# Kernel tuning notes

Measured on AMD Instinct MI355X. Metric: run time of the kernel, lower is better.

Reference implementation:

```python
import jax, jax.numpy as jnp
import numpy as np

N, T, IN, HID, ST, NL, OUT = 256, 2048, 6, 128, 64, 2, 6
LAY = IN + HID  # LMSCCell layer_size = input_size + hidden_size


def setup_inputs() -> dict:
    key = jax.random.key(0)
    ks = jax.random.split(key, 8)

    def w(k, shape, fan_in):
        return jax.random.normal(k, shape, jnp.float32) / np.sqrt(fan_in).astype(np.float32)

    return {
        "X": jax.random.normal(ks[0], (N, T, IN), jnp.float32),
        "H0": jax.random.normal(ks[1], (N, ST), jnp.float32),
        # NL gated layers (layer_size -> layer_size), stored stacked, weights as (in, out)
        "Wg1": w(ks[2], (NL, LAY, LAY), LAY), "bg1": jnp.zeros((NL, LAY), jnp.float32),
        "Wg2": w(ks[3], (NL, LAY, LAY), LAY), "bg2": jnp.zeros((NL, LAY), jnp.float32),
        # final pair: alpha (exp) and beta (tanh), layer_size -> hidden
        "Wa": w(ks[4], (LAY, HID), LAY), "ba": jnp.zeros((HID,), jnp.float32),
        "Wb": w(ks[5], (LAY, HID), LAY), "bb": jnp.zeros((HID,), jnp.float32),
        # hstate: Linear(state_size -> hidden) producing S0
        "Wh": w(ks[6], (ST, HID), ST), "bh": jnp.zeros((HID,), jnp.float32),
        # sstate2: Linear(hidden -> out_size)
        "Wo": w(ks[7], (HID, OUT), HID), "bo": jnp.zeros((OUT,), jnp.float32),
    }


def reference(X, H0, Wg1, bg1, Wg2, bg2, Wa, ba, Wb, bb, Wh, bh, Wo, bo):
    # hstate: initial hidden state for the LMSC recurrence
    S0 = H0 @ Wh + bh  # (N, HID)

    def step(H, x_t):
        # x_t: (N, IN); H: (N, HID)
        norm = jnp.linalg.norm(x_t, axis=1, keepdims=True)  # (N, 1)
        Lv = jnp.concatenate([x_t / norm, H], axis=1)       # (N, LAY)
        for i in range(NL):  # small fixed layer count, structurally distinct weights
            Lv = jnp.tanh(Lv @ Wg1[i] + bg1[i]) * jnp.tanh(Lv @ Wg2[i] + bg2[i])
        alpha = jnp.exp(Lv @ Wa + ba)   # (N, HID)
        beta = jnp.tanh(Lv @ Wb + bb)   # (N, HID)
        Hn = jnp.exp(-alpha * norm) * (H - beta) + beta
        return Hn, Hn

    _, Ys = jax.lax.scan(step, S0, jnp.swapaxes(X, 0, 1))  # (T, N, HID)
    Y = jnp.swapaxes(Ys, 0, 1)  # (N, T, HID)
    return Y @ Wo + bo          # (N, T, OUT)
```

## Files before the change

kernel.cpp:

```cpp
#include <hip/hip_runtime.h>

#define Nb   256
#define Tt   2048
#define INs  6
#define HID  128
#define STs  64
#define LAY  134
#define OUTs 6
#define NPAIR 67
#define NDW  68

typedef _Float16 h2 __attribute__((ext_vector_type(2)));
typedef __fp16  f16x2 __attribute__((ext_vector_type(2)));

__device__ __forceinline__ float exp2_fast(float x) {
#if __has_builtin(__builtin_amdgcn_exp2f)
    return __builtin_amdgcn_exp2f(x);
#else
    return exp2f(x);
#endif
}
__device__ __forceinline__ float rcp_fast(float x) {
#if __has_builtin(__builtin_amdgcn_rcpf)
    return __builtin_amdgcn_rcpf(x);
#else
    return 1.0f / x;
#endif
}
__device__ __forceinline__ float tanh_fast(float x) {
    float e = exp2_fast(x * 2.8853900817779268f);
    return 1.0f - 2.0f * rcp_fast(e + 1.0f);
}
__device__ __forceinline__ unsigned pack2(float a, float b) {
#if __has_builtin(__builtin_amdgcn_cvt_pkrtz)
    union { f16x2 h; unsigned u; } u;
    u.h = __builtin_amdgcn_cvt_pkrtz(a, b);
    return u.u;
#else
    union { h2 h; unsigned u; } u;
    u.h[0] = (_Float16)a; u.h[1] = (_Float16)b;
    return u.u;
#endif
}
__device__ __forceinline__ h2 as_h2(unsigned v) {
    union { unsigned u; h2 h; } u; u.u = v; return u.h;
}
__device__ __forceinline__ float dot2f(h2 a, h2 b, float c) {
#if __has_builtin(__builtin_amdgcn_fdot2)
    union { h2 h; f16x2 f; } ua, ub;
    ua.h = a; ub.h = b;
    return __builtin_amdgcn_fdot2(ua.f, ub.f, c, false);
#else
    return c + (float)a[0] * (float)b[0] + (float)a[1] * (float)b[1];
#endif
}

__device__ __forceinline__ void dotLv2(const unsigned* buf, const h2* w1, const h2* w2,
                                       float b1, float b2, float& o1, float& o2) {
    const uint4* b4 = (const uint4*)buf;
    float a0 = 0.f, a1 = 0.f, a2 = 0.f, a3 = 0.f;
    float c0 = 0.f, c1 = 0.f, c2 = 0.f, c3 = 0.f;
#pragma unroll
    for (int m = 0; m < 17; ++m) {
        uint4 v = b4[m];
        h2 vx = as_h2(v.x), vy = as_h2(v.y), vz = as_h2(v.z), vw = as_h2(v.w);
        a0 = dot2f(vx, w1[4*m+0], a0);  c0 = dot2f(vx, w2[4*m+0], c0);
        a1 = dot2f(vy, w1[4*m+1], a1);  c1 = dot2f(vy, w2[4*m+1], c1);
        a2 = dot2f(vz, w1[4*m+2], a2);  c2 = dot2f(vz, w2[4*m+2], c2);
        a3 = dot2f(vw, w1[4*m+3], a3);  c3 = dot2f(vw, w2[4*m+3], c3);
    }
    o1 = ((a0 + a1) + (a2 + a3)) + b1;
    o2 = ((c0 + c1) + (c2 + c3)) + b2;
}

__device__ __forceinline__ void do_proj(const float* Hrow, const float* wo0, const float* wo1,
                                        const float* bo6, float* outp, int l) {
    float hA = Hrow[2*l], hB = Hrow[2*l+1];
    float r[6];
#pragma unroll
    for (int o = 0; o < 6; ++o) r[o] = hA * wo0[o] + hB * wo1[o];
#pragma unroll
    for (int o = 0; o < 6; ++o) {
#pragma unroll
        for (int k = 1; k < 64; k <<= 1) r[o] += __shfl_xor(r[o], k, 64);
    }
    if (l == 0) {
#pragma unroll
        for (int o = 0; o < 6; ++o) outp[o] = r[o] + bo6[o];
    }
}

__global__ __launch_bounds__(512, 2)
void lmsc_kernel(const float* __restrict__ X,  const float* __restrict__ H0,
                 const float* __restrict__ Wg1, const float* __restrict__ bg1,
                 const float* __restrict__ Wg2, const float* __restrict__ bg2,
                 const float* __restrict__ Wa,  const float* __restrict__ ba,
                 const float* __restrict__ Wb,  const float* __restrict__ bb,
                 const float* __restrict__ Wh,  const float* __restrict__ bh,
                 const float* __restrict__ Wo,  const float* __restrict__ bo,
                 float* __restrict__ out)
{
    __shared__ float Xls[Tt * INs];
    __shared__ alignas(16) unsigned LvX[NDW];
    __shared__ alignas(16) unsigned LvB[NDW];
    __shared__ alignas(16) unsigned LvC[NDW];
    __shared__ float Hf[HID];
    __shared__ float H0l[STs];
    __shared__ float nrm[2], rnr[2];

    const int tid = threadIdx.x;
    const int n   = blockIdx.x;

    {
        const float4* Xg  = (const float4*)(X + (size_t)n * (Tt * INs));
        float4*       Xl4 = (float4*)Xls;
        for (int i = tid; i < (Tt * INs) / 4; i += 512) Xl4[i] = Xg[i];
    }
    if (tid < STs) H0l[tid] = H0[n * STs + tid];
    if (tid == 0) { LvX[NDW-1] = 0u; LvB[NDW-1] = 0u; LvC[NDW-1] = 0u; }

    h2 w1[NDW], w2[NDW];
    float b1 = 0.f, b2 = 0.f;
    {
        const float* Wp1 = nullptr; const float* Wp2 = nullptr; int od = LAY, j = 0;
        if (tid < 134) {
            Wp1 = Wg1;             Wp2 = Wg2;             j = tid;
            b1 = bg1[j];           b2 = bg2[j];
        } else if (tid >= 192 && tid < 326) {
            Wp1 = Wg1 + LAY*LAY;   Wp2 = Wg2 + LAY*LAY;   j = tid - 192;
            b1 = bg1[LAY + j];     b2 = bg2[LAY + j];
        } else if (tid >= 384) {
            Wp1 = Wa; Wp2 = Wb; od = HID;                 j = tid - 384;
            b1 = ba[j];            b2 = bb[j];
        }
        if (Wp1) {
            for (int m = 0; m < NPAIR; ++m) {
                h2 a; a[0] = (_Float16)Wp1[(2*m) * od + j]; a[1] = (_Float16)Wp1[(2*m+1) * od + j];
                h2 b; b[0] = (_Float16)Wp2[(2*m) * od + j]; b[1] = (_Float16)Wp2[(2*m+1) * od + j];
                w1[m] = a; w2[m] = b;
            }
        }
        h2 z; z[0] = (_Float16)0.f; z[1] = (_Float16)0.f;
        w1[NPAIR] = z; w2[NPAIR] = z;
    }
    float wo0[6], wo1[6], bo6[6];
    if (tid >= 384 && tid < 448) {
        int l = tid - 384;
#pragma unroll
        for (int o = 0; o < 6; ++o) {
            wo0[o] = Wo[(2*l)     * OUTs + o];
            wo1[o] = Wo[(2*l + 1) * OUTs + o];
            bo6[o] = bo[o];
        }
    }
    __syncthreads();

    float h = 0.f;
    if (tid >= 384) {
        int j = tid - 384;
        float s = bh[j];
        for (int k = 0; k < STs; ++k) s += H0l[k] * Wh[k * HID + j];
        h = s;
        Hf[j] = s;
        ((_Float16*)LvX)[6 + j] = (_Float16)s;
    }
    if (tid == 448 - 64) {}
    if (tid == 448) {
        float s = 0.f;
#pragma unroll
        for (int i = 0; i < 6; ++i) s += Xls[i] * Xls[i];
        float nv = sqrtf(s);
        float rn = rcp_fast(nv);
        nrm[0] = nv; rnr[0] = rn;
        LvX[0] = pack2(Xls[0]*rn, Xls[1]*rn);
        LvX[1] = pack2(Xls[2]*rn, Xls[3]*rn);
        LvX[2] = pack2(Xls[4]*rn, Xls[5]*rn);
    }
    __syncthreads();

    const float LOG2E = 1.4426950408889634f;

#pragma unroll 1
    for (int t = 0; t < Tt; ++t) {
        const int p = t & 1;
        if (tid < 134) {
            float s1, s2;
            dotLv2(LvX, w1, w2, b1, b2, s1, s2);
            float v = tanh_fast(s1) * tanh_fast(s2);
            ((_Float16*)LvB)[tid] = (_Float16)v;
        } else if (tid >= 384 && tid < 448) {
            if (t > 0)
                do_proj(Hf, wo0, wo1, bo6, out + ((size_t)n * Tt + (t - 1)) * OUTs, tid - 384);
        } else if (tid == 448 && (t + 1) < Tt) {
            const float* xp = &Xls[(t + 1) * INs];
            float s = 0.f;
#pragma unroll
            for (int i = 0; i < 6; ++i) s += xp[i] * xp[i];
            float nv = sqrtf(s);
            nrm[(t + 1) & 1] = nv;
            rnr[(t + 1) & 1] = rcp_fast(nv);
        }
        __syncthreads();
        if (tid >= 192 && tid < 326) {
            float s1, s2;
            dotLv2(LvB, w1, w2, b1, b2, s1, s2);
            float v = tanh_fast(s1) * tanh_fast(s2);
            ((_Float16*)LvC)[tid - 192] = (_Float16)v;
        } else if (tid == 0 && (t + 1) < Tt) {
            const float* xp = &Xls[(t + 1) * INs];
            float rn = rnr[(t + 1) & 1];
            LvX[0] = pack2(xp[0]*rn, xp[1]*rn);
            LvX[1] = pack2(xp[2]*rn, xp[3]*rn);
            LvX[2] = pack2(xp[4]*rn, xp[5]*rn);
        }
        __syncthreads();
        if (tid >= 384) {
            int j = tid - 384;
            float sA, sB;
            dotLv2(LvC, w1, w2, b1, b2, sA, sB);
            float a = exp2_fast(sA * LOG2E);
            float b = tanh_fast(sB);
            float e = exp2_fast(-a * nrm[p] * LOG2E);
            h = e * (h - b) + b;
            Hf[j] = h;
            ((_Float16*)LvX)[6 + j] = (_Float16)h;
        }
        __syncthreads();
    }
    if (tid >= 384 && tid < 448)
        do_proj(Hf, wo0, wo1, bo6, out + ((size_t)n * Tt + (Tt - 1)) * OUTs, tid - 384);
}

extern "C" void kernel_launch(void* const* d_in, const int* in_sizes, int n_in,
                              void* d_out, int out_size, void* d_ws, size_t ws_size,
                              hipStream_t stream) {
    const float* X   = (const float*)d_in[0];
    const float* H0  = (const float*)d_in[1];
    const float* Wg1 = (const float*)d_in[2];
    const float* bg1 = (const float*)d_in[3];
    const float* Wg2 = (const float*)d_in[4];
    const float* bg2 = (const float*)d_in[5];
    const float* Wa  = (const float*)d_in[6];
    const float* ba  = (const float*)d_in[7];
    const float* Wb  = (const float*)d_in[8];
    const float* bb  = (const float*)d_in[9];
    const float* Wh  = (const float*)d_in[10];
    const float* bh  = (const float*)d_in[11];
    const float* Wo  = (const float*)d_in[12];
    const float* bo  = (const float*)d_in[13];
    float* out = (float*)d_out;

    hipLaunchKernelGGL(lmsc_kernel, dim3(Nb), dim3(512), 0, stream,
                       X, H0, Wg1, bg1, Wg2, bg2, Wa, ba, Wb, bb, Wh, bh, Wo, bo, out);
}
```

Before: 3.537 ms.

## Split each gated dot-product pair across two threads with 1024-thread blocks

Each output neuron's two weight columns (tanh gate pair, or alpha/beta) now go to two adjacent lanes instead of one thread. Each lane holds half the weights, packed into f16x8 registers, and the pair is combined with a lane shuffle. The block grows from 512 to 1024 threads, which halves the serial dot-product length per thread on the recurrent critical path and cuts register pressure. In exchange it adds a shuffle, more idle lanes, and barrier cost over twice as many waves.

```diff
diff --git a/kernel.cpp b/kernel.cpp
--- a/kernel.cpp
+++ b/kernel.cpp
@@ -12,6 +12,7 @@
 
 typedef _Float16 h2 __attribute__((ext_vector_type(2)));
 typedef __fp16  f16x2 __attribute__((ext_vector_type(2)));
+typedef __fp16  f16x8 __attribute__((ext_vector_type(8)));
 
 __device__ __forceinline__ float exp2_fast(float x) {
 #if __has_builtin(__builtin_amdgcn_exp2f)
@@ -42,35 +43,43 @@
     return u.u;
 #endif
 }
-__device__ __forceinline__ h2 as_h2(unsigned v) {
-    union { unsigned u; h2 h; } u; u.u = v; return u.h;
-}
-__device__ __forceinline__ float dot2f(h2 a, h2 b, float c) {
+__device__ __forceinline__ float dot2p(unsigned av, f16x2 wv, float c) {
+    union { unsigned u; f16x2 f; } ua; ua.u = av;
 #if __has_builtin(__builtin_amdgcn_fdot2)
-    union { h2 h; f16x2 f; } ua, ub;
-    ua.h = a; ub.h = b;
-    return __builtin_amdgcn_fdot2(ua.f, ub.f, c, false);
-#else
-    return c + (float)a[0] * (float)b[0] + (float)a[1] * (float)b[1];
-#endif
-}
-
-__device__ __forceinline__ void dotLv2(const unsigned* buf, const h2* w1, const h2* w2,
-                                       float b1, float b2, float& o1, float& o2) {
-    const uint4* b4 = (const uint4*)buf;
-    float a0 = 0.f, a1 = 0.f, a2 = 0.f, a3 = 0.f;
-    float c0 = 0.f, c1 = 0.f, c2 = 0.f, c3 = 0.f;
-#pragma unroll
-    for (int m = 0; m < 17; ++m) {
-        uint4 v = b4[m];
-        h2 vx = as_h2(v.x), vy = as_h2(v.y), vz = as_h2(v.z), vw = as_h2(v.w);
-        a0 = dot2f(vx, w1[4*m+0], a0);  c0 = dot2f(vx, w2[4*m+0], c0);
-        a1 = dot2f(vy, w1[4*m+1], a1);  c1 = dot2f(vy, w2[4*m+1], c1);
-        a2 = dot2f(vz, w1[4*m+2], a2);  c2 = dot2f(vz, w2[4*m+2], c2);
-        a3 = dot2f(vw, w1[4*m+3], a3);  c3 = dot2f(vw, w2[4*m+3], c3);
-    }
-    o1 = ((a0 + a1) + (a2 + a3)) + b1;
-    o2 = ((c0 + c1) + (c2 + c3)) + b2;
+    return __builtin_amdgcn_fdot2(ua.f, wv, c, false);
+#else
+    return c + (float)ua.f[0] * (float)wv[0] + (float)ua.f[1] * (float)wv[1];
+#endif
+}
+
+#define WR17(M) M(0) M(1) M(2) M(3) M(4) M(5) M(6) M(7) M(8) M(9) M(10) M(11) M(12) M(13) M(14) M(15) M(16)
+
+#define DECLW(k) f16x8 w##k = {};
+
+#define LOADW(k) { \
+    f16x8 tmp; \
+    _Pragma("unroll") \
+    for (int q = 0; q < 8; ++q) { \
+        int r = 8 * (k) + q; \
+        float f = (r < LAY) ? Wp[r * od + j] : 0.f; \
+        tmp[q] = (__fp16)f; \
+    } \
+    w##k = tmp; \
+}
+
+#define DOT4(k) { \
+    uint4 v = b4[k]; \
+    a0 = dot2p(v.x, __builtin_shufflevector(w##k, w##k, 0, 1), a0); \
+    a1 = dot2p(v.y, __builtin_shufflevector(w##k, w##k, 2, 3), a1); \
+    a2 = dot2p(v.z, __builtin_shufflevector(w##k, w##k, 4, 5), a2); \
+    a3 = dot2p(v.w, __builtin_shufflevector(w##k, w##k, 6, 7), a3); \
+}
+
+#define DO_DOT(bufname, sres) { \
+    const uint4* b4 = (const uint4*)(bufname); \
+    float a0 = 0.f, a1 = 0.f, a2 = 0.f, a3 = 0.f; \
+    WR17(DOT4) \
+    sres = ((a0 + a1) + (a2 + a3)); \
 }
 
 __device__ __forceinline__ void do_proj(const float* Hrow, const float* wo0, const float* wo1,
@@ -90,7 +99,7 @@
     }
 }
 
-__global__ __launch_bounds__(512, 2)
+__global__ __launch_bounds__(1024, 4)
 void lmsc_kernel(const float* __restrict__ X,  const float* __restrict__ H0,
                  const float* __restrict__ Wg1, const float* __restrict__ bg1,
                  const float* __restrict__ Wg2, const float* __restrict__ bg2,
@@ -111,41 +120,41 @@
     const int tid = threadIdx.x;
     const int n   = blockIdx.x;
 
+    const bool isL1 = tid < 268;
+    const bool isL2 = (tid >= 320) & (tid < 588);
+    const bool isAB = (tid >= 640) & (tid < 896);
+    const bool isPJ = (tid >= 896) & (tid < 960);
+
     {
         const float4* Xg  = (const float4*)(X + (size_t)n * (Tt * INs));
         float4*       Xl4 = (float4*)Xls;
-        for (int i = tid; i < (Tt * INs) / 4; i += 512) Xl4[i] = Xg[i];
+        for (int i = tid; i < (Tt * INs) / 4; i += 1024) Xl4[i] = Xg[i];
     }
     if (tid < STs) H0l[tid] = H0[n * STs + tid];
-    if (tid == 0) { LvX[NDW-1] = 0u; LvB[NDW-1] = 0u; LvC[NDW-1] = 0u; }
-
-    h2 w1[NDW], w2[NDW];
-    float b1 = 0.f, b2 = 0.f;
+    if (tid == 1021) { LvX[NDW-1] = 0u; LvB[NDW-1] = 0u; LvC[NDW-1] = 0u; }
+
+    WR17(DECLW)
+    float bias = 0.f;
     {
-        const float* Wp1 = nullptr; const float* Wp2 = nullptr; int od = LAY, j = 0;
-        if (tid < 134) {
-            Wp1 = Wg1;             Wp2 = Wg2;             j = tid;
-            b1 = bg1[j];           b2 = bg2[j];
-        } else if (tid >= 192 && tid < 326) {
-            Wp1 = Wg1 + LAY*LAY;   Wp2 = Wg2 + LAY*LAY;   j = tid - 192;
-            b1 = bg1[LAY + j];     b2 = bg2[LAY + j];
-        } else if (tid >= 384) {
-            Wp1 = Wa; Wp2 = Wb; od = HID;                 j = tid - 384;
-            b1 = ba[j];            b2 = bb[j];
-        }
-        if (Wp1) {
-            for (int m = 0; m < NPAIR; ++m) {
-                h2 a; a[0] = (_Float16)Wp1[(2*m) * od + j]; a[1] = (_Float16)Wp1[(2*m+1) * od + j];
-                h2 b; b[0] = (_Float16)Wp2[(2*m) * od + j]; b[1] = (_Float16)Wp2[(2*m+1) * od + j];
-                w1[m] = a; w2[m] = b;
-            }
-        }
-        h2 z; z[0] = (_Float16)0.f; z[1] = (_Float16)0.f;
-        w1[NPAIR] = z; w2[NPAIR] = z;
+        const float* Wp = nullptr; int od = LAY, j = 0;
+        if (isL1) {
+            j = tid >> 1;
+            Wp = (tid & 1) ? Wg2 : Wg1;
+            bias = ((tid & 1) ? bg2 : bg1)[j];
+        } else if (isL2) {
+            j = (tid - 320) >> 1;
+            Wp = ((tid & 1) ? Wg2 : Wg1) + LAY * LAY;
+            bias = ((tid & 1) ? bg2 : bg1)[LAY + j];
+        } else if (isAB) {
+            j = (tid - 640) >> 1;
+            Wp = (tid & 1) ? Wb : Wa;  od = HID;
+            bias = ((tid & 1) ? bb : ba)[j];
+        }
+        if (Wp) { WR17(LOADW) }
     }
     float wo0[6], wo1[6], bo6[6];
-    if (tid >= 384 && tid < 448) {
-        int l = tid - 384;
+    if (isPJ) {
+        int l = tid - 896;
 #pragma unroll
         for (int o = 0; o < 6; ++o) {
             wo0[o] = Wo[(2*l)     * OUTs + o];
@@ -156,16 +165,15 @@
     __syncthreads();
 
     float h = 0.f;
-    if (tid >= 384) {
-        int j = tid - 384;
+    if (isAB && !(tid & 1)) {
+        int j = (tid - 640) >> 1;
         float s = bh[j];
         for (int k = 0; k < STs; ++k) s += H0l[k] * Wh[k * HID + j];
         h = s;
         Hf[j] = s;
         ((_Float16*)LvX)[6 + j] = (_Float16)s;
     }
-    if (tid == 448 - 64) {}
-    if (tid == 448) {
+    if (tid == 1022) {
         float s = 0.f;
 #pragma unroll
         for (int i = 0; i < 6; ++i) s += Xls[i] * Xls[i];
@@ -183,15 +191,15 @@
 #pragma unroll 1
     for (int t = 0; t < Tt; ++t) {
         const int p = t & 1;
-        if (tid < 134) {
-            float s1, s2;
-            dotLv2(LvX, w1, w2, b1, b2, s1, s2);
-            float v = tanh_fast(s1) * tanh_fast(s2);
-            ((_Float16*)LvB)[tid] = (_Float16)v;
-        } else if (tid >= 384 && tid < 448) {
+        if (isL1) {
+            float s; DO_DOT(LvX, s); s += bias;
+            float tn = tanh_fast(s);
+            float to = __shfl_xor(tn, 1, 64);
+            if (!(tid & 1)) ((_Float16*)LvB)[tid >> 1] = (_Float16)(tn * to);
+        } else if (isPJ) {
             if (t > 0)
-                do_proj(Hf, wo0, wo1, bo6, out + ((size_t)n * Tt + (t - 1)) * OUTs, tid - 384);
-        } else if (tid == 448 && (t + 1) < Tt) {
+                do_proj(Hf, wo0, wo1, bo6, out + ((size_t)n * Tt + (t - 1)) * OUTs, tid - 896);
+        } else if (tid == 1022 && (t + 1) < Tt) {
             const float* xp = &Xls[(t + 1) * INs];
             float s = 0.f;
 #pragma unroll
@@ -201,12 +209,12 @@
             rnr[(t + 1) & 1] = rcp_fast(nv);
         }
         __syncthreads();
-        if (tid >= 192 && tid < 326) {
-            float s1, s2;
-            dotLv2(LvB, w1, w2, b1, b2, s1, s2);
-            float v = tanh_fast(s1) * tanh_fast(s2);
-            ((_Float16*)LvC)[tid - 192] = (_Float16)v;
-        } else if (tid == 0 && (t + 1) < Tt) {
+        if (isL2) {
+            float s; DO_DOT(LvB, s); s += bias;
+            float tn = tanh_fast(s);
+            float to = __shfl_xor(tn, 1, 64);
+            if (!(tid & 1)) ((_Float16*)LvC)[(tid - 320) >> 1] = (_Float16)(tn * to);
+        } else if (tid == 1023 && (t + 1) < Tt) {
             const float* xp = &Xls[(t + 1) * INs];
             float rn = rnr[(t + 1) & 1];
             LvX[0] = pack2(xp[0]*rn, xp[1]*rn);
@@ -214,21 +222,23 @@
             LvX[2] = pack2(xp[4]*rn, xp[5]*rn);
         }
         __syncthreads();
-        if (tid >= 384) {
-            int j = tid - 384;
-            float sA, sB;
-            dotLv2(LvC, w1, w2, b1, b2, sA, sB);
-            float a = exp2_fast(sA * LOG2E);
-            float b = tanh_fast(sB);
-            float e = exp2_fast(-a * nrm[p] * LOG2E);
-            h = e * (h - b) + b;
-            Hf[j] = h;
-            ((_Float16*)LvX)[6 + j] = (_Float16)h;
+        if (isAB) {
+            float s; DO_DOT(LvC, s); s += bias;
+            float bown = tanh_fast(s);
+            float beta = __shfl_xor(bown, 1, 64);
+            if (!(tid & 1)) {
+                int j = (tid - 640) >> 1;
+                float alpha = exp2_fast(s * LOG2E);
+                float e = exp2_fast(-alpha * nrm[p] * LOG2E);
+                h = e * (h - beta) + beta;
+                Hf[j] = h;
+                ((_Float16*)LvX)[6 + j] = (_Float16)h;
+            }
         }
         __syncthreads();
     }
-    if (tid >= 384 && tid < 448)
-        do_proj(Hf, wo0, wo1, bo6, out + ((size_t)n * Tt + (Tt - 1)) * OUTs, tid - 384);
+    if (isPJ)
+        do_proj(Hf, wo0, wo1, bo6, out + ((size_t)n * Tt + (Tt - 1)) * OUTs, tid - 896);
 }
 
 extern "C" void kernel_launch(void* const* d_in, const int* in_sizes, int n_in,
@@ -250,6 +260,6 @@
     const float* bo  = (const float*)d_in[13];
     float* out = (float*)d_out;
 
-    hipLaunchKernelGGL(lmsc_kernel, dim3(Nb), dim3(512), 0, stream,
+    hipLaunchKernelGGL(lmsc_kernel, dim3(Nb), dim3(1024), 0, stream,
                        X, H0, Wg1, bg1, Wg2, bg2, Wa, ba, Wb, bb, Wh, bh, Wo, bo, out);
 }
```

Result: faster. 3.378 ms (-4.5%).
